# Performance work log

Measured on AMD Instinct MI355X. Metric: run time of the kernel, lower is better.

## Reference

```python
import jax, jax.numpy as jnp
import numpy as np

TEMP = 0.0005

def conv1d(x, w, b):
    # x: [B, Cin, T], w: [Cout, Cin, K] -> [B, Cout, T] with SAME padding
    out = jax.lax.conv_general_dilated(x, w, (1,), 'SAME', dimension_numbers=('NCH', 'OIH', 'NCH'))
    return out + b[None, :, None]

def setup_inputs() -> dict:
    key = jax.random.key(0)
    ks = jax.random.split(key, 24)
    B, Cs, T1 = 16, 80, 1000   # spec channels / mel frames
    Ct, T2 = 512, 200          # text channels / phonemes
    Ca, G = 80, 256            # attention channels / speaker embedding
    n = lambda i, shape: jax.random.normal(ks[i], shape, jnp.float32)
    w = lambda i, shape: n(i, shape) * 0.05
    return {
        'queries': n(0, (B, Cs, T1)),
        'keys': n(1, (B, Ct, T2)),
        'mask': jnp.ones((B, T2), jnp.int32),
        'attn_prior': jax.random.uniform(ks[2], (B, T1, T2), jnp.float32),
        'g': n(3, (B, G)),
        # key_proj: Conv(Ct -> 2Ct, k=3) -> ReLU -> Conv(2Ct -> Ca, k=1)
        'wk1': w(4, (2 * Ct, Ct, 3)), 'bk1': jnp.zeros((2 * Ct,), jnp.float32),
        'wk2': w(5, (Ca, 2 * Ct, 1)), 'bk2': jnp.zeros((Ca,), jnp.float32),
        # query_proj: Conv(Cs -> 2Cs, k=3) -> ReLU -> Conv(2Cs -> Cs, k=1) -> ReLU -> Conv(Cs -> Ca, k=1)
        'wq1': w(6, (2 * Cs, Cs, 3)), 'bq1': jnp.zeros((2 * Cs,), jnp.float32),
        'wq2': w(7, (Cs, 2 * Cs, 1)), 'bq2': jnp.zeros((Cs,), jnp.float32),
        'wq3': w(8, (Ca, Cs, 1)), 'bq3': jnp.zeros((Ca,), jnp.float32),
        # speaker projections (LinearNorm): gin -> n_text_channels / n_spec_channels
        'w_kspk': w(9, (Ct, G)), 'b_kspk': jnp.zeros((Ct,), jnp.float32),
        'w_qspk': w(10, (Cs, G)), 'b_qspk': jnp.zeros((Cs,), jnp.float32),
    }

def reference(queries, keys, mask, attn_prior, g, wk1, bk1, wk2, bk2, wq1, bq1, wq2, bq2, wq3, bq3, w_kspk, b_kspk, w_qspk, b_qspk):
    # speaker conditioning: same projected vector added at every time step
    keys = keys + (g @ w_kspk.T + b_kspk)[:, :, None]
    queries = queries + (g @ w_qspk.T + b_qspk)[:, :, None]
    # projections
    k_enc = conv1d(jax.nn.relu(conv1d(keys, wk1, bk1)), wk2, bk2)              # [B, Ca, T2]
    q = jax.nn.relu(conv1d(queries, wq1, bq1))
    q = jax.nn.relu(conv1d(q, wq2, bq2))
    q_enc = conv1d(q, wq3, bq3)                                                # [B, Ca, T1]
    # squared L2 distance via GEMM trick: |q|^2 + |k|^2 - 2 q.k  (same math as broadcast diff)
    q2 = jnp.sum(q_enc * q_enc, axis=1)[:, :, None]                            # [B, T1, 1]
    k2 = jnp.sum(k_enc * k_enc, axis=1)[:, None, :]                            # [B, 1, T2]
    qk = jnp.einsum('bct,bcs->bts', q_enc, k_enc)                              # [B, T1, T2]
    attn = (-TEMP * (q2 + k2 - 2.0 * qk))[:, None]                             # [B, 1, T1, T2]
    attn = jax.nn.log_softmax(attn, axis=3) + jnp.log(attn_prior[:, None] + 1e-8)
    attn_logprob = attn
    neg_inf = jnp.where(mask[:, None, None, :] == 0, -jnp.inf, 0.0)
    attn = jax.nn.softmax(attn + neg_inf, axis=3)
    return attn, attn_logprob
```

## Files before the change

### kernel.cpp

```cpp
#include <hip/hip_runtime.h>
#include <hip/hip_bf16.h>
#include <math.h>

#define NB 16
#define CS 80
#define T1 1000
#define CT 512
#define T2 200
#define CA 80
#define GD 256
#define C2T 1024
#define C2S 160
#define TEMP_F 0.0005f

typedef __attribute__((ext_vector_type(8))) short short8;
typedef __attribute__((ext_vector_type(4))) float floatx4;

__device__ __forceinline__ short f2bf(float x) {
    unsigned u = __builtin_bit_cast(unsigned, x);
    unsigned r = (u + 0x7fffu + ((u >> 16) & 1u)) >> 16;
    return (short)r;
}
__device__ __forceinline__ float bf2f(short s) {
    unsigned u = ((unsigned)(unsigned short)s) << 16;
    return __builtin_bit_cast(float, u);
}

template <int COUT, int CIN, int KW, int COP, int CINP>
__device__ __forceinline__ void wpack_body(const float* __restrict__ w,
                                           short* __restrict__ wp, int bid) {
    constexpr int NC32 = CINP / 32;
    constexpr int NFRAG = (COP / 16) * KW * NC32;
    int gid = bid * 256 + threadIdx.x;
    int frag = gid >> 6, lane = gid & 63;
    if (frag >= NFRAG) return;
    int co16 = frag / (KW * NC32), rem = frag - co16 * (KW * NC32);
    int k = rem / NC32, ci32 = rem - k * NC32;
    int co = co16 * 16 + (lane & 15);
    int ci = ci32 * 32 + (lane >> 4) * 8;
    short8 v;
#pragma unroll
    for (int j = 0; j < 8; j++) {
        float f = 0.f;
        if (co < COUT && ci + j < CIN) f = w[((size_t)co * CIN + ci + j) * KW + k];
        v[j] = f2bf(f);
    }
    *(short8*)(wp + (size_t)frag * 512 + lane * 8) = v;
}

template <int C, int T>
__device__ __forceinline__ void addspkT_body(const float* __restrict__ in,
                                             const float* __restrict__ g,
                                             const float* __restrict__ w_spk,
                                             const float* __restrict__ b_spk,
                                             short* __restrict__ outT,
                                             float* sm, int bx, int by, int b) {
    float* spkS = sm;
    float* S = sm + 32;
    const int t0 = bx * 64, c0 = by * 32;
    const int tid = threadIdx.x;
    int cl = tid >> 3, part = tid & 7;
    int c = c0 + cl;
    float s = 0.f;
    if (c < C) {
        const float* wr = w_spk + (size_t)c * GD;
        const float* gr = g + b * GD;
        int j0 = part * 32;
#pragma unroll
        for (int j = 0; j < 32; j++) s += gr[j0 + j] * wr[j0 + j];
    }
    s += __shfl_xor(s, 1, 64); s += __shfl_xor(s, 2, 64); s += __shfl_xor(s, 4, 64);
    if (part == 0) spkS[cl] = s + ((c < C) ? b_spk[c] : 0.f);
    __syncthreads();
    for (int i = tid; i < 32 * 64; i += 256) {
        int cll = i >> 6, tl = i & 63;
        int gc = c0 + cll, gt = t0 + tl;
        float v = 0.f;
        if (gc < C && gt < T) v = in[((size_t)b * C + gc) * T + gt] + spkS[cll];
        S[cll * 65 + tl] = v;
    }
    __syncthreads();
    for (int i = tid; i < 64 * 32; i += 256) {
        int tl = i >> 5, cll = i & 31;
        int gt = t0 + tl, gc = c0 + cll;
        if (gc < C && gt < T) outT[((size_t)b * T + gt) * C + gc] = f2bf(S[cll * 65 + tl]);
    }
}

__global__ __launch_bounds__(256) void prep_kernel(
    const float* __restrict__ keys, const float* __restrict__ queries, const float* __restrict__ g,
    const float* __restrict__ wk1, const float* __restrict__ wq1, const float* __restrict__ wk2,
    const float* __restrict__ wq2, const float* __restrict__ wq3,
    const float* __restrict__ w_kspk, const float* __restrict__ b_kspk,
    const float* __restrict__ w_qspk, const float* __restrict__ b_qspk,
    short* __restrict__ wk1p, short* __restrict__ wq1p, short* __restrict__ wk2p,
    short* __restrict__ wq2p, short* __restrict__ wq3p,
    short* __restrict__ xkT, short* __restrict__ xqT) {
    __shared__ float sm[32 + 32 * 65];
    int bid = blockIdx.x;
    if (bid < 768) { wpack_body<C2T, CT, 3, C2T, CT>(wk1, wk1p, bid); return; }
    bid -= 768;
    if (bid < 27) { wpack_body<C2S, CS, 3, 192, 96>(wq1, wq1p, bid); return; }
    bid -= 27;
    if (bid < 40) { wpack_body<CA, C2T, 1, 80, 1024>(wk2, wk2p, bid); return; }
    bid -= 40;
    if (bid < 7) { wpack_body<CA, C2S, 1, 80, 160>(wq2, wq2p, bid); return; }
    bid -= 7;
    if (bid < 4) { wpack_body<CA, CS, 1, 80, 96>(wq3, wq3p, bid); return; }
    bid -= 4;
    if (bid < 1024) {
        int bx = bid & 3, by = (bid >> 2) & 15, b = bid >> 6;
        addspkT_body<CT, T2>(keys, g, w_kspk, b_kspk, xkT, sm, bx, by, b);
        return;
    }
    bid -= 1024;
    {
        int bx = bid & 15, by = (bid >> 4) % 3, b = bid / 48;
        addspkT_body<CS, T1>(queries, g, w_qspk, b_qspk, xqT, sm, bx, by, b);
    }
}

template <int CIN, int COUT, int T, int KW, bool RELU, int CICH, int NC32T>
__device__ __forceinline__ void conv_body(const short* __restrict__ xT,
                                          const short* __restrict__ wp,
                                          const float* __restrict__ bias,
                                          short* __restrict__ outT,
                                          short* Xs, int bx, int by, int b) {
    constexpr int TT = 128, COT = 64;
    constexpr int PAD = KW / 2;
    constexpr int XROWS = TT + KW - 1;
    constexpr int PITCH = CICH + 8;
    constexpr int NPC = CICH / 8;
    constexpr int NC32 = CICH / 32;
    constexpr int CINP = NC32T * 32;
    constexpr int NCHK = CINP / CICH;
    constexpr int NPIECE = XROWS * NPC;
    constexpr int NLD = (NPIECE + 255) / 256;

    const int t0 = bx * TT, co0 = by * COT;
    const int tid = threadIdx.x, wave = tid >> 6, lane = tid & 63;
    const int quad = lane >> 4, l16 = lane & 15;
    const int wt = wave * 32;
    const int co16_0 = co0 >> 4;
    const short* xb = xT + (size_t)b * T * CIN;

    floatx4 acc[4][2];
#pragma unroll
    for (int mi = 0; mi < 4; mi++)
#pragma unroll
        for (int ni = 0; ni < 2; ni++) acc[mi][ni] = (floatx4){0.f, 0.f, 0.f, 0.f};

    for (int i = tid; i < NPIECE; i += 256) {
        int r = i / NPC, p = i - r * NPC;
        int t = t0 + r - PAD, ci = p * 8;
        uint4 v = {0u, 0u, 0u, 0u};
        if ((unsigned)t < (unsigned)T && ci + 8 <= CIN)
            v = *(const uint4*)(xb + (size_t)t * CIN + ci);
        *(uint4*)(Xs + r * PITCH + p * 8) = v;
    }
    __syncthreads();

    for (int kc = 0; kc < NCHK; kc++) {
        uint4 tmp[NLD];
        if (NCHK > 1 && kc + 1 < NCHK) {
            int ci0n = (kc + 1) * CICH;
#pragma unroll
            for (int ld = 0; ld < NLD; ld++) {
                int i = tid + ld * 256;
                tmp[ld] = (uint4){0u, 0u, 0u, 0u};
                if (i < NPIECE) {
                    int r = i / NPC, p = i - r * NPC;
                    int t = t0 + r - PAD, ci = ci0n + p * 8;
                    if ((unsigned)t < (unsigned)T && ci + 8 <= CIN)
                        tmp[ld] = *(const uint4*)(xb + (size_t)t * CIN + ci);
                }
            }
        }
        const short* Xb = Xs + (NCHK > 1 ? (kc & 1) : 0) * XROWS * PITCH;
#pragma unroll
        for (int k = 0; k < KW; k++) {
#pragma unroll
            for (int kk = 0; kk < NC32; kk++) {
                int ci32 = kc * NC32 + kk;
                short8 a[4];
#pragma unroll
                for (int mi = 0; mi < 4; mi++)
                    a[mi] = *(const short8*)(wp +
                        ((size_t)((co16_0 + mi) * KW + k) * NC32T + ci32) * 512 + lane * 8);
#pragma unroll
                for (int ni = 0; ni < 2; ni++) {
                    short8 bb = *(const short8*)(Xb + (wt + ni * 16 + l16 + k) * PITCH +
                                                 kk * 32 + quad * 8);
#pragma unroll
                    for (int mi = 0; mi < 4; mi++)
                        acc[mi][ni] = __builtin_amdgcn_mfma_f32_16x16x32_bf16(a[mi], bb,
                                                                              acc[mi][ni], 0, 0, 0);
                }
            }
        }
        if (NCHK > 1 && kc + 1 < NCHK) {
            short* Xn = Xs + ((kc + 1) & 1) * XROWS * PITCH;
#pragma unroll
            for (int ld = 0; ld < NLD; ld++) {
                int i = tid + ld * 256;
                if (i < NPIECE) {
                    int r = i / NPC, p = i - r * NPC;
                    *(uint4*)(Xn + r * PITCH + p * 8) = tmp[ld];
                }
            }
            __syncthreads();
        }
    }
#pragma unroll
    for (int mi = 0; mi < 4; mi++) {
        int cb = co0 + mi * 16 + quad * 4;
        if (cb < COUT) {
            float4 bv = *(const float4*)(bias + cb);
#pragma unroll
            for (int ni = 0; ni < 2; ni++) {
                int t = t0 + wt + ni * 16 + l16;
                if (t < T) {
                    float v0 = acc[mi][ni][0] + bv.x, v1 = acc[mi][ni][1] + bv.y;
                    float v2 = acc[mi][ni][2] + bv.z, v3 = acc[mi][ni][3] + bv.w;
                    if (RELU) {
                        v0 = fmaxf(v0, 0.f); v1 = fmaxf(v1, 0.f);
                        v2 = fmaxf(v2, 0.f); v3 = fmaxf(v3, 0.f);
                    }
                    ushort4 o;
                    o.x = (unsigned short)f2bf(v0); o.y = (unsigned short)f2bf(v1);
                    o.z = (unsigned short)f2bf(v2); o.w = (unsigned short)f2bf(v3);
                    *(ushort4*)(outT + ((size_t)b * T + t) * COUT + cb) = o;
                }
            }
        }
    }
}

__global__ __launch_bounds__(256, 2) void conv_kernel(
    const short* __restrict__ xkT, const short* __restrict__ wk1p,
    const float* __restrict__ bk1, short* __restrict__ kh1T,
    const short* __restrict__ xqT, const short* __restrict__ wq1p,
    const float* __restrict__ bq1, short* __restrict__ qh1T) {
    __shared__ short sm[18720];
    int bid = blockIdx.x;
    if (bid < 512) {
        int bx = bid & 1, by = (bid >> 1) & 15, b = bid >> 5;
        conv_body<CT, C2T, T2, 3, true, 64, 16>(xkT, wk1p, bk1, kh1T, sm, bx, by, b);
    } else {
        int r = bid - 512;
        int bx = r & 7, by = (r >> 3) % 3, b = r / 24;
        conv_body<CS, C2S, T1, 3, true, 96, 3>(xqT, wq1p, bq1, qh1T, sm, bx, by, b);
    }
}

__device__ __forceinline__ void kgemm_body(const short* __restrict__ xT,
                                           const short* __restrict__ wp,
                                           const float* __restrict__ bias,
                                           short* __restrict__ outT, short* sm, int bid) {
    constexpr int K = 1024, KCH = 128, PITCH = 136, NPC = 16, NCHK = 8;
    const int n0 = bid * 64;
    const int tid = threadIdx.x, wave = tid >> 6, lane = tid & 63;
    const int quad = lane >> 4, l16 = lane & 15;
    floatx4 acc[5];
#pragma unroll
    for (int mi = 0; mi < 5; mi++) acc[mi] = (floatx4){0.f, 0.f, 0.f, 0.f};

    for (int i = tid; i < 64 * NPC; i += 256) {
        int r = i / NPC, p = i - r * NPC;
        *(uint4*)(sm + r * PITCH + p * 8) = *(const uint4*)(xT + (size_t)(n0 + r) * K + p * 8);
    }
    __syncthreads();
    for (int kc = 0; kc < NCHK; kc++) {
        uint4 tmp[4];
        if (kc + 1 < NCHK) {
            int ci0 = (kc + 1) * KCH;
#pragma unroll
            for (int ld = 0; ld < 4; ld++) {
                int i = tid + ld * 256;
                int r = i / NPC, p = i - r * NPC;
                tmp[ld] = *(const uint4*)(xT + (size_t)(n0 + r) * K + ci0 + p * 8);
            }
        }
        const short* Xb = sm + (kc & 1) * 64 * PITCH;
#pragma unroll
        for (int kk = 0; kk < 4; kk++) {
            int ci32 = kc * 4 + kk;
            short8 bb = *(const short8*)(Xb + (wave * 16 + l16) * PITCH + kk * 32 + quad * 8);
#pragma unroll
            for (int mi = 0; mi < 5; mi++) {
                short8 a = *(const short8*)(wp + ((size_t)(mi * 32 + ci32)) * 512 + lane * 8);
                acc[mi] = __builtin_amdgcn_mfma_f32_16x16x32_bf16(a, bb, acc[mi], 0, 0, 0);
            }
        }
        if (kc + 1 < NCHK) {
            short* Xn = sm + ((kc + 1) & 1) * 64 * PITCH;
#pragma unroll
            for (int ld = 0; ld < 4; ld++) {
                int i = tid + ld * 256;
                int r = i / NPC, p = i - r * NPC;
                *(uint4*)(Xn + r * PITCH + p * 8) = tmp[ld];
            }
            __syncthreads();
        }
    }
    int n = n0 + wave * 16 + l16;
#pragma unroll
    for (int mi = 0; mi < 5; mi++) {
        int cb = mi * 16 + quad * 4;
        float4 bv = *(const float4*)(bias + cb);
        ushort4 o;
        o.x = (unsigned short)f2bf(acc[mi][0] + bv.x);
        o.y = (unsigned short)f2bf(acc[mi][1] + bv.y);
        o.z = (unsigned short)f2bf(acc[mi][2] + bv.z);
        o.w = (unsigned short)f2bf(acc[mi][3] + bv.w);
        *(ushort4*)(outT + (size_t)n * CA + cb) = o;
    }
}

__device__ __forceinline__ void qconv23_body(const short* __restrict__ h1,
                                             const short* __restrict__ w2p,
                                             const float* __restrict__ b2,
                                             const short* __restrict__ w3p,
                                             const float* __restrict__ b3,
                                             short* __restrict__ outT, short* sm, int bid) {
    constexpr int K1 = 160, P1 = 168, NPC1 = 20, P3 = 104;
    short* Xs = sm;
    short* Hs = sm + 64 * P1;
    const int n0 = bid * 64;
    const int tid = threadIdx.x, wave = tid >> 6, lane = tid & 63;
    const int quad = lane >> 4, l16 = lane & 15;

    for (int i = tid; i < 64 * NPC1; i += 256) {
        int r = i / NPC1, p = i - r * NPC1;
        *(uint4*)(Xs + r * P1 + p * 8) = *(const uint4*)(h1 + (size_t)(n0 + r) * K1 + p * 8);
    }
    if (tid < 128) *(uint4*)(Hs + (tid >> 1) * P3 + 80 + (tid & 1) * 8) = (uint4){0u, 0u, 0u, 0u};
    __syncthreads();

    floatx4 acc[5];
#pragma unroll
    for (int mi = 0; mi < 5; mi++) acc[mi] = (floatx4){0.f, 0.f, 0.f, 0.f};
#pragma unroll
    for (int kk = 0; kk < 5; kk++) {
        short8 bb = *(const short8*)(Xs + (wave * 16 + l16) * P1 + kk * 32 + quad * 8);
#pragma unroll
        for (int mi = 0; mi < 5; mi++) {
            short8 a = *(const short8*)(w2p + ((size_t)(mi * 5 + kk)) * 512 + lane * 8);
            acc[mi] = __builtin_amdgcn_mfma_f32_16x16x32_bf16(a, bb, acc[mi], 0, 0, 0);
        }
    }
#pragma unroll
    for (int mi = 0; mi < 5; mi++) {
        int cb = mi * 16 + quad * 4;
        float4 bv = *(const float4*)(b2 + cb);
        ushort4 o;
        o.x = (unsigned short)f2bf(fmaxf(acc[mi][0] + bv.x, 0.f));
        o.y = (unsigned short)f2bf(fmaxf(acc[mi][1] + bv.y, 0.f));
        o.z = (unsigned short)f2bf(fmaxf(acc[mi][2] + bv.z, 0.f));
        o.w = (unsigned short)f2bf(fmaxf(acc[mi][3] + bv.w, 0.f));
        *(ushort4*)(Hs + (wave * 16 + l16) * P3 + cb) = o;
    }
    __syncthreads();

    floatx4 acc3[5];
#pragma unroll
    for (int mi = 0; mi < 5; mi++) acc3[mi] = (floatx4){0.f, 0.f, 0.f, 0.f};
#pragma unroll
    for (int kk = 0; kk < 3; kk++) {
        short8 bb = *(const short8*)(Hs + (wave * 16 + l16) * P3 + kk * 32 + quad * 8);
#pragma unroll
        for (int mi = 0; mi < 5; mi++) {
            short8 a = *(const short8*)(w3p + ((size_t)(mi * 3 + kk)) * 512 + lane * 8);
            acc3[mi] = __builtin_amdgcn_mfma_f32_16x16x32_bf16(a, bb, acc3[mi], 0, 0, 0);
        }
    }
    int n = n0 + wave * 16 + l16;
#pragma unroll
    for (int mi = 0; mi < 5; mi++) {
        int cb = mi * 16 + quad * 4;
        float4 bv = *(const float4*)(b3 + cb);
        ushort4 o;
        o.x = (unsigned short)f2bf(acc3[mi][0] + bv.x);
        o.y = (unsigned short)f2bf(acc3[mi][1] + bv.y);
        o.z = (unsigned short)f2bf(acc3[mi][2] + bv.z);
        o.w = (unsigned short)f2bf(acc3[mi][3] + bv.w);
        *(ushort4*)(outT + (size_t)n * CA + cb) = o;
    }
}

__global__ __launch_bounds__(256, 2) void gemm_kernel(
    const short* __restrict__ kh1T, const short* __restrict__ wk2p,
    const float* __restrict__ bk2, short* __restrict__ k_encT,
    const short* __restrict__ qh1T, const short* __restrict__ wq2p,
    const float* __restrict__ bq2, const short* __restrict__ wq3p,
    const float* __restrict__ bq3, short* __restrict__ q_encT) {
    __shared__ short sm[17408];
    int bid = blockIdx.x;
    if (bid < 50) kgemm_body(kh1T, wk2p, bk2, k_encT, sm, bid);
    else qconv23_body(qh1T, wq2p, bq2, wq3p, bq3, q_encT, sm, bid - 50);
}

__device__ __forceinline__ float rmax16(float v) {
#pragma unroll
    for (int o = 1; o < 16; o <<= 1) v = fmaxf(v, __shfl_xor(v, o, 64));
    return v;
}
__device__ __forceinline__ float rsum16(float v) {
#pragma unroll
    for (int o = 1; o < 16; o <<= 1) v += __shfl_xor(v, o, 64);
    return v;
}

__global__ __launch_bounds__(256) void attn_kernel(const short* __restrict__ q_encT,
                                                   const short* __restrict__ k_encT,
                                                   const float* __restrict__ prior,
                                                   const int* __restrict__ mask,
                                                   float* __restrict__ out_attn,
                                                   float* __restrict__ out_logp) {
    constexpr int T2R = 208, PITCH = 104, NPC = 12;
    __shared__ short Kt[T2R * PITCH];
    __shared__ short Qs[64 * PITCH];
    __shared__ float k2s[T2R];
    __shared__ int msk[T2R];
    const int t10 = blockIdx.x * 64, b = blockIdx.y;
    const int tid = threadIdx.x;
    const int wave = tid >> 6, lane = tid & 63;
    const int quad = lane >> 4, l16 = lane & 15;

    for (int i = tid; i < T2R * NPC; i += 256) {
        int r = i / NPC, p = i - r * NPC;
        uint4 v = {0u, 0u, 0u, 0u};
        if (r < T2 && p < 10) v = *(const uint4*)(k_encT + ((size_t)b * T2 + r) * CA + p * 8);
        *(uint4*)(Kt + r * PITCH + p * 8) = v;
    }
    for (int i = tid; i < 64 * NPC; i += 256) {
        int r = i / NPC, p = i - r * NPC;
        int t1 = t10 + r;
        uint4 v = {0u, 0u, 0u, 0u};
        if (t1 < T1 && p < 10) v = *(const uint4*)(q_encT + ((size_t)b * T1 + t1) * CA + p * 8);
        *(uint4*)(Qs + r * PITCH + p * 8) = v;
    }
    if (tid < T2R) msk[tid] = (tid < T2) ? mask[b * T2 + tid] : 0;
    __syncthreads();
    for (int r = tid; r < T2R; r += 256) {
        float s = 0.f;
        for (int p = 0; p < NPC; p++) {
            short8 v = *(const short8*)(Kt + r * PITCH + p * 8);
#pragma unroll
            for (int j = 0; j < 8; j++) { float f = bf2f(v[j]); s += f * f; }
        }
        k2s[r] = s;
    }
    __syncthreads();

    floatx4 acc[13];
#pragma unroll
    for (int n = 0; n < 13; n++) acc[n] = (floatx4){0.f, 0.f, 0.f, 0.f};
#pragma unroll
    for (int kk = 0; kk < 3; kk++) {
        short8 a = *(const short8*)(Qs + (wave * 16 + l16) * PITCH + kk * 32 + quad * 8);
#pragma unroll
        for (int n = 0; n < 13; n++) {
            short8 bb = *(const short8*)(Kt + (n * 16 + l16) * PITCH + kk * 32 + quad * 8);
            acc[n] = __builtin_amdgcn_mfma_f32_16x16x32_bf16(a, bb, acc[n], 0, 0, 0);
        }
    }

#pragma unroll
    for (int r = 0; r < 4; r++) {
        int t1 = t10 + wave * 16 + quad * 4 + r;
        bool t1ok = t1 < T1;
        float s[13];
        float mx = -INFINITY;
#pragma unroll
        for (int n = 0; n < 13; n++) {
            int t2 = n * 16 + l16;
            float sv = -INFINITY;
            if (t2 < T2) sv = -TEMP_F * (k2s[t2] - 2.f * acc[n][r]);
            s[n] = sv;
            mx = fmaxf(mx, sv);
        }
        float m = rmax16(mx);
        float sume = 0.f;
#pragma unroll
        for (int n = 0; n < 13; n++) sume += (s[n] == -INFINITY) ? 0.f : __expf(s[n] - m);
        float logZ = __logf(rsum16(sume));
        float mx2 = -INFINITY;
#pragma unroll
        for (int n = 0; n < 13; n++) {
            int t2 = n * 16 + l16;
            float pr = 1.f;
            if (t1ok && t2 < T2) pr = prior[((size_t)b * T1 + t1) * T2 + t2];
            float lp = (t2 < T2) ? (s[n] - m - logZ + __logf(pr + 1e-8f)) : -INFINITY;
            s[n] = lp;
            float ms = (t2 < T2 && msk[t2] != 0) ? lp : -INFINITY;
            mx2 = fmaxf(mx2, ms);
        }
        float m2 = rmax16(mx2);
        float sume2 = 0.f;
        float e2v[13];
#pragma unroll
        for (int n = 0; n < 13; n++) {
            int t2 = n * 16 + l16;
            float ms = (t2 < T2 && msk[t2] != 0) ? s[n] : -INFINITY;
            float e = (ms == -INFINITY) ? 0.f : __expf(ms - m2);
            e2v[n] = e;
            sume2 += e;
        }
        float Z2 = rsum16(sume2);
        if (t1ok) {
#pragma unroll
            for (int n = 0; n < 13; n++) {
                int t2 = n * 16 + l16;
                if (t2 < T2) {
                    size_t o = ((size_t)b * T1 + t1) * T2 + t2;
                    out_attn[o] = e2v[n] / Z2;
                    out_logp[o] = s[n];
                }
            }
        }
    }
}

extern "C" void kernel_launch(void* const* d_in, const int* in_sizes, int n_in,
                              void* d_out, int out_size, void* d_ws, size_t ws_size,
                              hipStream_t stream) {
    const float* queries = (const float*)d_in[0];
    const float* keys    = (const float*)d_in[1];
    const int*   mask    = (const int*)d_in[2];
    const float* prior   = (const float*)d_in[3];
    const float* g       = (const float*)d_in[4];
    const float* wk1 = (const float*)d_in[5];
    const float* bk1 = (const float*)d_in[6];
    const float* wk2 = (const float*)d_in[7];
    const float* bk2 = (const float*)d_in[8];
    const float* wq1 = (const float*)d_in[9];
    const float* bq1 = (const float*)d_in[10];
    const float* wq2 = (const float*)d_in[11];
    const float* bq2 = (const float*)d_in[12];
    const float* wq3 = (const float*)d_in[13];
    const float* bq3 = (const float*)d_in[14];
    const float* w_kspk = (const float*)d_in[15];
    const float* b_kspk = (const float*)d_in[16];
    const float* w_qspk = (const float*)d_in[17];
    const float* b_qspk = (const float*)d_in[18];

    short* wsS   = (short*)d_ws;
    short* xkT   = wsS;
    short* xqT   = wsS + 1638400;
    short* wk1p  = wsS + 2918400;
    short* wq1p  = wsS + 4491264;
    short* wk2p  = wsS + 4546560;
    short* wq2p  = wsS + 4628480;
    short* wq3p  = wsS + 4641280;
    short* k_encT = wsS + 4648960;
    short* q_encT = wsS + 4904960;
    short* doS  = (short*)d_out;
    short* kh1T = doS;
    short* qh1T = doS + 3276800;

    prep_kernel<<<dim3(2638), dim3(256), 0, stream>>>(
        keys, queries, g, wk1, wq1, wk2, wq2, wq3,
        w_kspk, b_kspk, w_qspk, b_qspk,
        wk1p, wq1p, wk2p, wq2p, wq3p, xkT, xqT);
    conv_kernel<<<dim3(896), dim3(256), 0, stream>>>(xkT, wk1p, bk1, kh1T,
                                                     xqT, wq1p, bq1, qh1T);
    gemm_kernel<<<dim3(300), dim3(256), 0, stream>>>(kh1T, wk2p, bk2, k_encT,
                                                     qh1T, wq2p, bq2, wq3p, bq3, q_encT);
    float* out_attn = (float*)d_out;
    float* out_logp = out_attn + (size_t)NB * T1 * T2;
    attn_kernel<<<dim3(16, NB), dim3(256), 0, stream>>>(q_encT, k_encT, prior, mask,
                                                        out_attn, out_logp);
}
```

Before: 211.2 us.

## Fuse k-norm into key GEMM epilogue and stream attention operands from global

After: 190.5 us. 9.8% less time.

```diff
diff --git a/kernel.cpp b/kernel.cpp
--- a/kernel.cpp
+++ b/kernel.cpp
@@ -12,6 +12,7 @@
 #define C2T 1024
 #define C2S 160
 #define TEMP_F 0.0005f
+#define ENC_STR 96
 
 typedef __attribute__((ext_vector_type(8))) short short8;
 typedef __attribute__((ext_vector_type(4))) float floatx4;
@@ -20,10 +21,6 @@
     unsigned u = __builtin_bit_cast(unsigned, x);
     unsigned r = (u + 0x7fffu + ((u >> 16) & 1u)) >> 16;
     return (short)r;
-}
-__device__ __forceinline__ float bf2f(short s) {
-    unsigned u = ((unsigned)(unsigned short)s) << 16;
-    return __builtin_bit_cast(float, u);
 }
 
 template <int COUT, int CIN, int KW, int COP, int CINP>
@@ -256,7 +253,9 @@
 __device__ __forceinline__ void kgemm_body(const short* __restrict__ xT,
                                            const short* __restrict__ wp,
                                            const float* __restrict__ bias,
-                                           short* __restrict__ outT, short* sm, int bid) {
+                                           short* __restrict__ outT,
+                                           float* __restrict__ k2ws,
+                                           short* sm, int bid) {
     constexpr int K = 1024, KCH = 128, PITCH = 136, NPC = 16, NCHK = 8;
     const int n0 = bid * 64;
     const int tid = threadIdx.x, wave = tid >> 6, lane = tid & 63;
@@ -304,17 +303,23 @@
         }
     }
     int n = n0 + wave * 16 + l16;
+    float sq = 0.f;
 #pragma unroll
     for (int mi = 0; mi < 5; mi++) {
         int cb = mi * 16 + quad * 4;
         float4 bv = *(const float4*)(bias + cb);
+        float v0 = acc[mi][0] + bv.x, v1 = acc[mi][1] + bv.y;
+        float v2 = acc[mi][2] + bv.z, v3 = acc[mi][3] + bv.w;
+        sq += v0 * v0 + v1 * v1 + v2 * v2 + v3 * v3;
         ushort4 o;
-        o.x = (unsigned short)f2bf(acc[mi][0] + bv.x);
-        o.y = (unsigned short)f2bf(acc[mi][1] + bv.y);
-        o.z = (unsigned short)f2bf(acc[mi][2] + bv.z);
-        o.w = (unsigned short)f2bf(acc[mi][3] + bv.w);
-        *(ushort4*)(outT + (size_t)n * CA + cb) = o;
-    }
+        o.x = (unsigned short)f2bf(v0); o.y = (unsigned short)f2bf(v1);
+        o.z = (unsigned short)f2bf(v2); o.w = (unsigned short)f2bf(v3);
+        *(ushort4*)(outT + (size_t)n * ENC_STR + cb) = o;
+    }
+    if (quad < 2) *(uint4*)(outT + (size_t)n * ENC_STR + 80 + quad * 8) = (uint4){0u, 0u, 0u, 0u};
+    sq += __shfl_xor(sq, 16, 64);
+    sq += __shfl_xor(sq, 32, 64);
+    if (quad == 0) k2ws[n] = sq;
 }
 
 __device__ __forceinline__ void qconv23_body(const short* __restrict__ h1,
@@ -384,19 +389,20 @@
         o.y = (unsigned short)f2bf(acc3[mi][1] + bv.y);
         o.z = (unsigned short)f2bf(acc3[mi][2] + bv.z);
         o.w = (unsigned short)f2bf(acc3[mi][3] + bv.w);
-        *(ushort4*)(outT + (size_t)n * CA + cb) = o;
-    }
+        *(ushort4*)(outT + (size_t)n * ENC_STR + cb) = o;
+    }
+    if (quad < 2) *(uint4*)(outT + (size_t)n * ENC_STR + 80 + quad * 8) = (uint4){0u, 0u, 0u, 0u};
 }
 
 __global__ __launch_bounds__(256, 2) void gemm_kernel(
     const short* __restrict__ kh1T, const short* __restrict__ wk2p,
-    const float* __restrict__ bk2, short* __restrict__ k_encT,
+    const float* __restrict__ bk2, short* __restrict__ k_encT, float* __restrict__ k2ws,
     const short* __restrict__ qh1T, const short* __restrict__ wq2p,
     const float* __restrict__ bq2, const short* __restrict__ wq3p,
     const float* __restrict__ bq3, short* __restrict__ q_encT) {
     __shared__ short sm[17408];
     int bid = blockIdx.x;
-    if (bid < 50) kgemm_body(kh1T, wk2p, bk2, k_encT, sm, bid);
+    if (bid < 50) kgemm_body(kh1T, wk2p, bk2, k_encT, k2ws, sm, bid);
     else qconv23_body(qh1T, wq2p, bq2, wq3p, bq3, q_encT, sm, bid - 50);
 }
 
@@ -413,109 +419,86 @@
 
 __global__ __launch_bounds__(256) void attn_kernel(const short* __restrict__ q_encT,
                                                    const short* __restrict__ k_encT,
+                                                   const float* __restrict__ k2ws,
                                                    const float* __restrict__ prior,
                                                    const int* __restrict__ mask,
                                                    float* __restrict__ out_attn,
                                                    float* __restrict__ out_logp) {
-    constexpr int T2R = 208, PITCH = 104, NPC = 12;
-    __shared__ short Kt[T2R * PITCH];
-    __shared__ short Qs[64 * PITCH];
-    __shared__ float k2s[T2R];
-    __shared__ int msk[T2R];
     const int t10 = blockIdx.x * 64, b = blockIdx.y;
-    const int tid = threadIdx.x;
-    const int wave = tid >> 6, lane = tid & 63;
+    const int tid = threadIdx.x, wave = tid >> 6, lane = tid & 63;
     const int quad = lane >> 4, l16 = lane & 15;
 
-    for (int i = tid; i < T2R * NPC; i += 256) {
-        int r = i / NPC, p = i - r * NPC;
-        uint4 v = {0u, 0u, 0u, 0u};
-        if (r < T2 && p < 10) v = *(const uint4*)(k_encT + ((size_t)b * T2 + r) * CA + p * 8);
-        *(uint4*)(Kt + r * PITCH + p * 8) = v;
-    }
-    for (int i = tid; i < 64 * NPC; i += 256) {
-        int r = i / NPC, p = i - r * NPC;
-        int t1 = t10 + r;
-        uint4 v = {0u, 0u, 0u, 0u};
-        if (t1 < T1 && p < 10) v = *(const uint4*)(q_encT + ((size_t)b * T1 + t1) * CA + p * 8);
-        *(uint4*)(Qs + r * PITCH + p * 8) = v;
-    }
-    if (tid < T2R) msk[tid] = (tid < T2) ? mask[b * T2 + tid] : 0;
-    __syncthreads();
-    for (int r = tid; r < T2R; r += 256) {
-        float s = 0.f;
-        for (int p = 0; p < NPC; p++) {
-            short8 v = *(const short8*)(Kt + r * PITCH + p * 8);
-#pragma unroll
-            for (int j = 0; j < 8; j++) { float f = bf2f(v[j]); s += f * f; }
-        }
-        k2s[r] = s;
-    }
-    __syncthreads();
+    float k2v[13]; int mskv[13];
+#pragma unroll
+    for (int n = 0; n < 13; n++) {
+        int t2 = n * 16 + l16, t2c = t2 < T2 ? t2 : T2 - 1;
+        k2v[n] = k2ws[b * T2 + t2c];
+        mskv[n] = (t2 < T2) ? mask[b * T2 + t2] : 0;
+    }
+    const int t1base = t10 + wave * 16 + quad * 4;
+    float pr[4][13];
+#pragma unroll
+    for (int r = 0; r < 4; r++) {
+        int t1 = t1base + r, t1c = t1 < T1 ? t1 : T1 - 1;
+#pragma unroll
+        for (int n = 0; n < 13; n++) {
+            int t2 = n * 16 + l16, t2c = t2 < T2 ? t2 : T2 - 1;
+            pr[r][n] = prior[((size_t)b * T1 + t1c) * T2 + t2c];
+        }
+    }
 
     floatx4 acc[13];
 #pragma unroll
     for (int n = 0; n < 13; n++) acc[n] = (floatx4){0.f, 0.f, 0.f, 0.f};
+    const short* qb = q_encT + ((size_t)(b * T1 + t10 + wave * 16 + l16)) * ENC_STR + quad * 8;
+    const short* kb = k_encT + ((size_t)(b * T2 + l16)) * ENC_STR + quad * 8;
 #pragma unroll
     for (int kk = 0; kk < 3; kk++) {
-        short8 a = *(const short8*)(Qs + (wave * 16 + l16) * PITCH + kk * 32 + quad * 8);
+        short8 a = *(const short8*)(qb + kk * 32);
 #pragma unroll
         for (int n = 0; n < 13; n++) {
-            short8 bb = *(const short8*)(Kt + (n * 16 + l16) * PITCH + kk * 32 + quad * 8);
+            short8 bb = *(const short8*)(kb + (size_t)n * 16 * ENC_STR + kk * 32);
             acc[n] = __builtin_amdgcn_mfma_f32_16x16x32_bf16(a, bb, acc[n], 0, 0, 0);
         }
     }
 
 #pragma unroll
     for (int r = 0; r < 4; r++) {
-        int t1 = t10 + wave * 16 + quad * 4 + r;
+        int t1 = t1base + r;
         bool t1ok = t1 < T1;
-        float s[13];
-        float mx = -INFINITY;
+        float s[13], u[13];
+        float mx = -INFINITY, mxu = -INFINITY;
 #pragma unroll
         for (int n = 0; n < 13; n++) {
             int t2 = n * 16 + l16;
-            float sv = -INFINITY;
-            if (t2 < T2) sv = -TEMP_F * (k2s[t2] - 2.f * acc[n][r]);
+            float sv = (t2 < T2) ? TEMP_F * (2.f * acc[n][r] - k2v[n]) : -INFINITY;
             s[n] = sv;
+            float uv = (t2 < T2) ? sv + __logf(pr[r][n] + 1e-8f) : -INFINITY;
+            u[n] = uv;
             mx = fmaxf(mx, sv);
+            mxu = fmaxf(mxu, (mskv[n] != 0) ? uv : -INFINITY);
         }
         float m = rmax16(mx);
-        float sume = 0.f;
-#pragma unroll
-        for (int n = 0; n < 13; n++) sume += (s[n] == -INFINITY) ? 0.f : __expf(s[n] - m);
-        float logZ = __logf(rsum16(sume));
-        float mx2 = -INFINITY;
+        float m2 = rmax16(mxu);
+        float se = 0.f, se2 = 0.f;
+        float e2v[13];
 #pragma unroll
         for (int n = 0; n < 13; n++) {
-            int t2 = n * 16 + l16;
-            float pr = 1.f;
-            if (t1ok && t2 < T2) pr = prior[((size_t)b * T1 + t1) * T2 + t2];
-            float lp = (t2 < T2) ? (s[n] - m - logZ + __logf(pr + 1e-8f)) : -INFINITY;
-            s[n] = lp;
-            float ms = (t2 < T2 && msk[t2] != 0) ? lp : -INFINITY;
-            mx2 = fmaxf(mx2, ms);
-        }
-        float m2 = rmax16(mx2);
-        float sume2 = 0.f;
-        float e2v[13];
-#pragma unroll
-        for (int n = 0; n < 13; n++) {
-            int t2 = n * 16 + l16;
-            float ms = (t2 < T2 && msk[t2] != 0) ? s[n] : -INFINITY;
-            float e = (ms == -INFINITY) ? 0.f : __expf(ms - m2);
-            e2v[n] = e;
-            sume2 += e;
-        }
-        float Z2 = rsum16(sume2);
+            se += (s[n] == -INFINITY) ? 0.f : __expf(s[n] - m);
+            float e2 = (mskv[n] != 0) ? __expf(u[n] - m2) : 0.f;
+            e2v[n] = e2;
+            se2 += e2;
+        }
+        float logZ = __logf(rsum16(se));
+        float invZ2 = 1.f / rsum16(se2);
         if (t1ok) {
 #pragma unroll
             for (int n = 0; n < 13; n++) {
                 int t2 = n * 16 + l16;
                 if (t2 < T2) {
                     size_t o = ((size_t)b * T1 + t1) * T2 + t2;
-                    out_attn[o] = e2v[n] / Z2;
-                    out_logp[o] = s[n];
+                    out_attn[o] = e2v[n] * invZ2;
+                    out_logp[o] = u[n] - m - logZ;
                 }
             }
         }
@@ -554,7 +537,8 @@
     short* wq2p  = wsS + 4628480;
     short* wq3p  = wsS + 4641280;
     short* k_encT = wsS + 4648960;
-    short* q_encT = wsS + 4904960;
+    short* q_encT = wsS + 4957696;
+    float* k2ws  = (float*)d_ws + 3248384;
     short* doS  = (short*)d_out;
     short* kh1T = doS;
     short* qh1T = doS + 3276800;
@@ -565,10 +549,10 @@
         wk1p, wq1p, wk2p, wq2p, wq3p, xkT, xqT);
     conv_kernel<<<dim3(896), dim3(256), 0, stream>>>(xkT, wk1p, bk1, kh1T,
                                                      xqT, wq1p, bq1, qh1T);
-    gemm_kernel<<<dim3(300), dim3(256), 0, stream>>>(kh1T, wk2p, bk2, k_encT,
+    gemm_kernel<<<dim3(300), dim3(256), 0, stream>>>(kh1T, wk2p, bk2, k_encT, k2ws,
                                                      qh1T, wq2p, bq2, wq3p, bq3, q_encT);
     float* out_attn = (float*)d_out;
     float* out_logp = out_attn + (size_t)NB * T1 * T2;
-    attn_kernel<<<dim3(16, NB), dim3(256), 0, stream>>>(q_encT, k_encT, prior, mask,
+    attn_kernel<<<dim3(16, NB), dim3(256), 0, stream>>>(q_encT, k_encT, k2ws, prior, mask,
                                                         out_attn, out_logp);
 }
```
